# Kernel optimization log

Hardware: AMD Instinct MI355X
Metric: run time of the kernel (lower is better)

Reference implementation:

```python
import jax, jax.numpy as jnp
import numpy as np

HID = 256
STYLE_DIM = 64
NUM_STYLES = 8
IN_DIM = 3 + STYLE_DIM


def setup_inputs() -> dict:
    key = jax.random.key(0)
    ks = jax.random.split(key, 12)
    B, H, W = 2, 512, 512
    rgb = jax.random.uniform(ks[0], (B, 3, H, W), dtype=jnp.float32)
    style_idx = jax.random.randint(ks[1], (B,), 0, NUM_STYLES, dtype=jnp.int32)
    # style embedding table (torch init: normal std=0.01)
    emb_table = 0.01 * jax.random.normal(ks[2], (NUM_STYLES, STYLE_DIM), dtype=jnp.float32)
    # kaiming-normal (fan_in, relu gain sqrt(2)) weights stored as [in, out]
    def kaiming(k, fan_in, fan_out):
        std = np.sqrt(2.0 / fan_in)
        return std * jax.random.normal(k, (fan_in, fan_out), dtype=jnp.float32)
    W0 = kaiming(ks[3], IN_DIM, HID); b0 = jnp.zeros((HID,), jnp.float32)
    W1 = kaiming(ks[4], HID, HID);    b1 = jnp.zeros((HID,), jnp.float32)
    W2 = kaiming(ks[5], HID, HID);    b2 = jnp.zeros((HID,), jnp.float32)
    W3 = kaiming(ks[6], HID, 3);      b3 = jnp.zeros((3,), jnp.float32)
    return {"rgb": rgb, "style_idx": style_idx, "emb_table": emb_table,
            "W0": W0, "b0": b0, "W1": W1, "b1": b1,
            "W2": W2, "b2": b2, "W3": W3, "b3": b3}


def reference(rgb, style_idx, emb_table, W0, b0, W1, b1, W2, b2, W3, b3):
    B, C, H, W_ = rgb.shape  # CHW image input
    # [B,3,H,W] -> [B*H*W, 3]
    rgb_flat = jnp.transpose(rgb, (0, 2, 3, 1)).reshape(-1, 3)
    # style embedding lookup, broadcast per pixel
    emb = emb_table[style_idx]                              # [B, style_dim]
    emb = jnp.broadcast_to(emb[:, None, :], (B, H * W_, STYLE_DIM)).reshape(-1, STYLE_DIM)
    x = jnp.concatenate([rgb_flat, emb], axis=-1)           # [N, 67]
    gelu = lambda t: jax.nn.gelu(t, approximate=False)      # torch nn.GELU default (erf)
    x = gelu(x @ W0 + b0)
    x = gelu(x @ W1 + b1)
    x = gelu(x @ W2 + b2)
    out_flat = jax.nn.sigmoid(x @ W3 + b3)                  # [N, 3]
    out = out_flat.reshape(B, H, W_, 3).transpose(0, 3, 1, 2)
    return out
```

## Files before the change

kernel.cpp:

```cpp
#include <hip/hip_runtime.h>

#define HW  (512*512)

typedef _Float16 half8  __attribute__((__vector_size__(16)));
typedef _Float16 half4  __attribute__((__vector_size__(8)));
typedef _Float16 half2_t __attribute__((__vector_size__(4)));
typedef float    floatx4 __attribute__((__vector_size__(16)));
typedef float    floatx2 __attribute__((__vector_size__(8)));

__device__ __forceinline__ float gelu_f(float x){
    float x2 = x * x;
    float q  = __builtin_fmaf(x2, -0.1029432f, -2.3022079f);
    float e  = __builtin_amdgcn_exp2f(x * q);
    return x * __builtin_amdgcn_rcpf(1.0f + e);
}

__device__ __forceinline__ float sigmoid_f(float x){
    float e = __builtin_amdgcn_exp2f(-1.44269504f * x);
    return __builtin_amdgcn_rcpf(1.0f + e);
}

__device__ __forceinline__ float glut_eval(const float* gl, float x){
    float p = __builtin_fmaf(x, 128.0f, 1024.0f);
    p = fminf(fmaxf(p, 0.0f), 2040.0f);
    unsigned off = ((unsigned)p) & 0xFFFFFFF8u;
    floatx2 ab = *(const floatx2*)((const char*)gl + off);
    return __builtin_fmaf(ab[0], x, ab[1]);
}


__global__ void prep_all(const float* __restrict__ W1, const float* __restrict__ W2,
                         const float* __restrict__ W3, const float* __restrict__ emb,
                         const int* __restrict__ sidx, const float* __restrict__ W0,
                         const float* __restrict__ b0,
                         _Float16* __restrict__ wp, float* __restrict__ c0){
    __shared__ float ld[32][68];
    int blk = blockIdx.x;
    int tid = threadIdx.x;
    if (blk < 64){
        int mat = blk >> 5;
        int g   = blk & 31;
        int ks  = g >> 2;
        int ntq = g & 3;
        const float* W = mat ? W2 : W1;
        int row = tid >> 3;
        int c8  = (tid & 7) * 8;
        const float* src = &W[(ks*32 + row)*256 + ntq*64 + c8];
        *(floatx4*)&ld[row][c8]     = *(const floatx4*)src;
        *(floatx4*)&ld[row][c8 + 4] = *(const floatx4*)(src + 4);
        __syncthreads();
        int lane = tid & 63;
        int nt_l = tid >> 6;
        half8 h;
        #pragma unroll
        for (int j = 0; j < 8; j++)
            h[j] = (_Float16)ld[(lane >> 4)*8 + j][nt_l*16 + (lane & 15)];
        _Float16* dst = wp + mat*65536 + (ks*16 + ntq*4 + nt_l)*512 + lane*8;
        *(half8*)dst = h;
    } else if (blk < 80){
        int i    = (blk - 64)*256 + tid;
        int j    = i & 7;
        int lane = (i >> 3) & 63;
        int ks   = i >> 9;
        int k = ks*32 + ((lane >> 4) << 3) + j;
        int n = lane & 15;
        wp[131072 + i] = (_Float16)((n < 3) ? W3[k*3 + n] : 0.0f);
    } else {
        int b = blk - 80;
        int s = sidx[b];
        float acc = b0[tid];
        #pragma unroll 8
        for (int d = 0; d < 64; d++)
            acc = fmaf(emb[s*64 + d], W0[(3 + d)*256 + tid], acc);
        c0[b*256 + tid] = acc;
    }
}

__global__ __launch_bounds__(256, 4)
void nilut_main(const float* __restrict__ rgb,
                const float* __restrict__ W0,
                const float* __restrict__ b1v,
                const float* __restrict__ b2v,
                const float* __restrict__ b3v,
                const _Float16* __restrict__ wp,
                const float* __restrict__ c0,
                float* __restrict__ out){
    __shared__ __align__(16) _Float16 act[64 * 256];
    __shared__ __align__(16) float    w0s[1024];
    __shared__ __align__(16) float    rgbs[192];
    __shared__ __align__(16) float    glut[512];

    const int tid = threadIdx.x;
    const int wg  = blockIdx.x;
    const int pixbase = wg * 64;
    const int b   = pixbase >> 18;
    const int hw0 = pixbase & (HW - 1);

    #pragma unroll
    for (int r = 0; r < 4; r++){
        int q = r*256 + tid;
        w0s[q] = (q < 768) ? W0[q] : c0[b*256 + (q - 768)];
    }
    if (tid < 192){
        int c = tid >> 6, row = tid & 63;
        rgbs[tid] = rgb[b*3*HW + c*HW + hw0 + row];
    }
    {
        float x0 = -8.0f + (float)tid * 0.0625f;
        float g0 = gelu_f(x0);
        float g1 = gelu_f(x0 + 0.0625f);
        float a  = (g1 - g0) * 16.0f;
        float bb = __builtin_fmaf(-a, x0, g0);
        floatx2 ab = {a, bb};
        *(floatx2*)&glut[2*tid] = ab;
    }
    __syncthreads();

    {
        int ng = tid & 31;
        int rg = tid >> 5;
        floatx2 cw2[4][4];
        #pragma unroll
        for (int p = 0; p < 4; p++){
            const floatx2* w2 = (const floatx2*)&w0s[p*256 + ng*8];
            #pragma unroll
            for (int q = 0; q < 4; q++) cw2[p][q] = w2[q];
        }
        #pragma unroll
        for (int hf = 0; hf < 2; hf++){
            floatx4 rv[3];
            #pragma unroll
            for (int c = 0; c < 3; c++)
                rv[c] = *(const floatx4*)&rgbs[c*64 + rg*8 + hf*4];
            #pragma unroll
            for (int r4 = 0; r4 < 4; r4++){
                int row = rg*8 + hf*4 + r4;
                floatx2 rr2 = {rv[0][r4], rv[0][r4]};
                floatx2 gg2 = {rv[1][r4], rv[1][r4]};
                floatx2 bb2 = {rv[2][r4], rv[2][r4]};
                half8 v;
                #pragma unroll
                for (int j2 = 0; j2 < 4; j2++){
                    floatx2 z2 = rr2*cw2[0][j2] + (gg2*cw2[1][j2] + (bb2*cw2[2][j2] + cw2[3][j2]));
                    half2_t g = __builtin_amdgcn_cvt_pkrtz(glut_eval(glut, z2[0]),
                                                           glut_eval(glut, z2[1]));
                    v[2*j2]   = g[0];
                    v[2*j2+1] = g[1];
                }
                *(half8*)&act[row*256 + ((ng ^ (row & 7)) << 3)] = v;
            }
        }
    }
    __syncthreads();

    const int lane = tid & 63;
    const int wv   = tid >> 6;
    const int ln15 = lane & 15;
    const int quad = lane >> 4;
    const int qr   = quad * 4;
    const int sx   = ln15 & 7;
    const int qx8  = (quad ^ (sx & 3)) * 8;
    const int kb32 = ((sx >> 2) & 1) << 5;

    int pbq[4];
    #pragma unroll
    for (int pt = 0; pt < 4; pt++)
        pbq[pt] = (pt*16 + ln15)*256 + qx8;

    const int qh = quad >> 1, qs = (quad & 1) * 4;
    int eb[4];
    #pragma unroll
    for (int pt = 0; pt < 4; pt++)
        eb[pt] = (pt*16 + ln15)*256 + qs;

    const _Float16* wl  = wp;
    const float* bias   = b1v;
    #pragma unroll 1
    for (int L = 0; L < 2; L++){
        floatx4 acc[4][4];
        #pragma unroll
        for (int mtl = 0; mtl < 4; mtl++){
            floatx4 bv = *(const floatx4*)&bias[(wv*4 + mtl)*16 + qr];
            #pragma unroll
            for (int pt = 0; pt < 4; pt++)
                acc[pt][mtl] = bv;
        }

        const half8* wp8 = (const half8*)wl;
        #pragma unroll 2
        for (int ks = 0; ks < 8; ks++){
            int t = (ks << 5) ^ kb32;
            half8 bfr[4];
            #pragma unroll
            for (int pt = 0; pt < 4; pt++)
                bfr[pt] = *(const half8*)&act[pbq[pt] + t];
            #pragma unroll
            for (int mtl = 0; mtl < 4; mtl++){
                half8 af = wp8[(ks*16 + wv*4 + mtl)*64 + lane];
                #pragma unroll
                for (int pt = 0; pt < 4; pt++)
                    acc[pt][mtl] = __builtin_amdgcn_mfma_f32_16x16x32_f16(af, bfr[pt], acc[pt][mtl], 0, 0, 0);
            }
        }
        __syncthreads();
        #pragma unroll
        for (int mtl = 0; mtl < 4; mtl++){
            int cx = (((wv*4 + mtl)*2 + qh) ^ sx) << 3;
            #pragma unroll
            for (int pt = 0; pt < 4; pt++){
                floatx4 v = acc[pt][mtl];
                half2_t g01 = __builtin_amdgcn_cvt_pkrtz(glut_eval(glut, v[0]),
                                                         glut_eval(glut, v[1]));
                half2_t g23 = __builtin_amdgcn_cvt_pkrtz(glut_eval(glut, v[2]),
                                                         glut_eval(glut, v[3]));
                half4 h;
                h[0] = g01[0]; h[1] = g01[1]; h[2] = g23[0]; h[3] = g23[1];
                *(half4*)&act[eb[pt] + cx] = h;
            }
        }
        __syncthreads();
        wl = wp + 65536;
        bias = b2v;
    }

    {
        const half8* wp8 = (const half8*)(wp + 131072);
        floatx4 ac = (floatx4){0.f,0.f,0.f,0.f};
        int pb = (wv*16 + ln15)*256 + qx8;
        #pragma unroll
        for (int ks = 0; ks < 8; ks++){
            half8 bfr = *(const half8*)&act[pb + ((ks << 5) ^ kb32)];
            half8 af  = wp8[ks*64 + lane];
            ac = __builtin_amdgcn_mfma_f32_16x16x32_f16(af, bfr, ac, 0, 0, 0);
        }
        if (quad == 0){
            #pragma unroll
            for (int r = 0; r < 3; r++)
                w0s[r*64 + wv*16 + ln15] = sigmoid_f(ac[r] + b3v[r]);
        }
        __syncthreads();
        if (tid < 48){
            int c  = tid >> 4;
            int i2 = tid & 15;
            float4* dst = (float4*)(out + (b*3 + c)*HW + hw0);
            dst[i2] = ((float4*)(w0s + c*64))[i2];
        }
    }
}

extern "C" void kernel_launch(void* const* d_in, const int* in_sizes, int n_in,
                              void* d_out, int out_size, void* d_ws, size_t ws_size,
                              hipStream_t stream){
    const float* rgb = (const float*)d_in[0];
    const int*  sidx = (const int*) d_in[1];
    const float* emb = (const float*)d_in[2];
    const float* W0  = (const float*)d_in[3];
    const float* b0  = (const float*)d_in[4];
    const float* W1  = (const float*)d_in[5];
    const float* b1  = (const float*)d_in[6];
    const float* W2  = (const float*)d_in[7];
    const float* b2  = (const float*)d_in[8];
    const float* W3  = (const float*)d_in[9];
    const float* b3  = (const float*)d_in[10];
    float* out = (float*)d_out;

    _Float16* wp = (_Float16*)d_ws;
    float*    c0 = (float*)((char*)d_ws + 270336);

    int n_pix = in_sizes[0] / 3;
    prep_all<<<82, 256, 0, stream>>>(W1, W2, W3, emb, sidx, W0, b0, wp, c0);
    nilut_main<<<n_pix / 64, 256, 0, stream>>>(rgb, W0, b1, b2, b3, wp, c0, out);
}
```

Baseline: 247.4 us.

## Retile hidden-layer MFMA per wave, swizzle W0 LDS, use exact GELU in layer 0

Each wave now covers 2 pixel tiles by 8 output tiles instead of 4 by 4. That halves activation fragment reads from LDS per wave but doubles the weight fragments fetched from global or L2 per wave. W0 stored in LDS gets an XOR swizzle, and the reads are adjusted to match, to cut bank conflicts when building layer-0 weights. Layer 0 switches from the piecewise-linear GELU lookup to the direct exp/rcp GELU approximation, which moves work from LDS lookups to ALU.

```diff
diff --git a/kernel.cpp b/kernel.cpp
--- a/kernel.cpp
+++ b/kernel.cpp
@@ -99,7 +99,7 @@
     #pragma unroll
     for (int r = 0; r < 4; r++){
         int q = r*256 + tid;
-        w0s[q] = (q < 768) ? W0[q] : c0[b*256 + (q - 768)];
+        w0s[q ^ ((q >> 4) & 6)] = (q < 768) ? W0[q] : c0[b*256 + (q - 768)];
     }
     if (tid < 192){
         int c = tid >> 6, row = tid & 63;
@@ -119,12 +119,14 @@
     {
         int ng = tid & 31;
         int rg = tid >> 5;
+        int s2 = (ng >> 2) & 3;
         floatx2 cw2[4][4];
         #pragma unroll
         for (int p = 0; p < 4; p++){
-            const floatx2* w2 = (const floatx2*)&w0s[p*256 + ng*8];
-            #pragma unroll
-            for (int q = 0; q < 4; q++) cw2[p][q] = w2[q];
+            const float* bp = &w0s[p*256 + ng*8];
+            #pragma unroll
+            for (int q = 0; q < 4; q++)
+                cw2[p][q] = *(const floatx2*)&bp[2*(q ^ s2)];
         }
         #pragma unroll
         for (int hf = 0; hf < 2; hf++){
@@ -142,8 +144,7 @@
                 #pragma unroll
                 for (int j2 = 0; j2 < 4; j2++){
                     floatx2 z2 = rr2*cw2[0][j2] + (gg2*cw2[1][j2] + (bb2*cw2[2][j2] + cw2[3][j2]));
-                    half2_t g = __builtin_amdgcn_cvt_pkrtz(glut_eval(glut, z2[0]),
-                                                           glut_eval(glut, z2[1]));
+                    half2_t g = __builtin_amdgcn_cvt_pkrtz(gelu_f(z2[0]), gelu_f(z2[1]));
                     v[2*j2]   = g[0];
                     v[2*j2+1] = g[1];
                 }
@@ -155,6 +156,8 @@
 
     const int lane = tid & 63;
     const int wv   = tid >> 6;
+    const int pw   = wv & 1;
+    const int nw   = wv >> 1;
     const int ln15 = lane & 15;
     const int quad = lane >> 4;
     const int qr   = quad * 4;
@@ -162,60 +165,56 @@
     const int qx8  = (quad ^ (sx & 3)) * 8;
     const int kb32 = ((sx >> 2) & 1) << 5;
 
-    int pbq[4];
+    int pbq[2];
     #pragma unroll
-    for (int pt = 0; pt < 4; pt++)
-        pbq[pt] = (pt*16 + ln15)*256 + qx8;
+    for (int t2 = 0; t2 < 2; t2++)
+        pbq[t2] = ((pw*2 + t2)*16 + ln15)*256 + qx8;
 
     const int qh = quad >> 1, qs = (quad & 1) * 4;
-    int eb[4];
+    int eb[2];
     #pragma unroll
-    for (int pt = 0; pt < 4; pt++)
-        eb[pt] = (pt*16 + ln15)*256 + qs;
+    for (int t2 = 0; t2 < 2; t2++)
+        eb[t2] = ((pw*2 + t2)*16 + ln15)*256 + qs;
 
     const _Float16* wl  = wp;
     const float* bias   = b1v;
     #pragma unroll 1
     for (int L = 0; L < 2; L++){
-        floatx4 acc[4][4];
-        #pragma unroll
-        for (int mtl = 0; mtl < 4; mtl++){
-            floatx4 bv = *(const floatx4*)&bias[(wv*4 + mtl)*16 + qr];
-            #pragma unroll
-            for (int pt = 0; pt < 4; pt++)
-                acc[pt][mtl] = bv;
+        floatx4 acc[2][8];
+        #pragma unroll
+        for (int mtl = 0; mtl < 8; mtl++){
+            floatx4 bv = *(const floatx4*)&bias[(nw*8 + mtl)*16 + qr];
+            acc[0][mtl] = bv;
+            acc[1][mtl] = bv;
         }
 
         const half8* wp8 = (const half8*)wl;
         #pragma unroll 2
         for (int ks = 0; ks < 8; ks++){
             int t = (ks << 5) ^ kb32;
-            half8 bfr[4];
-            #pragma unroll
-            for (int pt = 0; pt < 4; pt++)
-                bfr[pt] = *(const half8*)&act[pbq[pt] + t];
-            #pragma unroll
-            for (int mtl = 0; mtl < 4; mtl++){
-                half8 af = wp8[(ks*16 + wv*4 + mtl)*64 + lane];
-                #pragma unroll
-                for (int pt = 0; pt < 4; pt++)
-                    acc[pt][mtl] = __builtin_amdgcn_mfma_f32_16x16x32_f16(af, bfr[pt], acc[pt][mtl], 0, 0, 0);
+            half8 bfr0 = *(const half8*)&act[pbq[0] + t];
+            half8 bfr1 = *(const half8*)&act[pbq[1] + t];
+            #pragma unroll
+            for (int mtl = 0; mtl < 8; mtl++){
+                half8 af = wp8[(ks*16 + nw*8 + mtl)*64 + lane];
+                acc[0][mtl] = __builtin_amdgcn_mfma_f32_16x16x32_f16(af, bfr0, acc[0][mtl], 0, 0, 0);
+                acc[1][mtl] = __builtin_amdgcn_mfma_f32_16x16x32_f16(af, bfr1, acc[1][mtl], 0, 0, 0);
             }
         }
         __syncthreads();
         #pragma unroll
-        for (int mtl = 0; mtl < 4; mtl++){
-            int cx = (((wv*4 + mtl)*2 + qh) ^ sx) << 3;
-            #pragma unroll
-            for (int pt = 0; pt < 4; pt++){
-                floatx4 v = acc[pt][mtl];
+        for (int mtl = 0; mtl < 8; mtl++){
+            int cx = (((nw*8 + mtl)*2 + qh) ^ sx) << 3;
+            #pragma unroll
+            for (int t2 = 0; t2 < 2; t2++){
+                floatx4 v = acc[t2][mtl];
                 half2_t g01 = __builtin_amdgcn_cvt_pkrtz(glut_eval(glut, v[0]),
                                                          glut_eval(glut, v[1]));
                 half2_t g23 = __builtin_amdgcn_cvt_pkrtz(glut_eval(glut, v[2]),
                                                          glut_eval(glut, v[3]));
                 half4 h;
                 h[0] = g01[0]; h[1] = g01[1]; h[2] = g23[0]; h[3] = g23[1];
-                *(half4*)&act[eb[pt] + cx] = h;
+                *(half4*)&act[eb[t2] + cx] = h;
             }
         }
         __syncthreads();
```

Measured after the change: 273.3 us. 10.5% more time.
